# Kernel tuning notes

Measured on AMD Instinct MI355X. Metric: run time of the kernel, lower is better.

## Reference

```python
import jax, jax.numpy as jnp
import numpy as np

N_NODES = 100000
N_EDGES = 1600000
HIDDEN = 128
N_FILTERS = 64
CUTOFF = 8.0
BN_EPS = 1e-3  # keras BatchNormalization default epsilon


def setup_inputs() -> dict:
    key = jax.random.key(0)
    ks = jax.random.split(key, 12)
    x = jax.random.normal(ks[0], (N_NODES, HIDDEN), dtype=jnp.float32)
    edge_index = jax.random.randint(ks[1], (2, N_EDGES), 0, N_NODES, dtype=jnp.int32)
    edge_weight = jax.random.uniform(ks[2], (N_EDGES,), dtype=jnp.float32) * CUTOFF
    edge_attr = jax.random.uniform(ks[3], (N_EDGES, 1), dtype=jnp.float32)
    s = 0.05
    # filter_net: Dense(1->64, tanh), Dense(64->64)
    Wf1 = jax.random.normal(ks[4], (1, N_FILTERS), dtype=jnp.float32) * s
    bf1 = jnp.zeros((N_FILTERS,), jnp.float32)
    Wf2 = jax.random.normal(ks[5], (N_FILTERS, N_FILTERS), dtype=jnp.float32) * s
    bf2 = jnp.zeros((N_FILTERS,), jnp.float32)
    # interaction_net: Dense(128->128, softplus), Dense(128->128)
    Wi1 = jax.random.normal(ks[6], (HIDDEN, HIDDEN), dtype=jnp.float32) * s
    bi1 = jnp.zeros((HIDDEN,), jnp.float32)
    Wi2 = jax.random.normal(ks[7], (HIDDEN, HIDDEN), dtype=jnp.float32) * s
    bi2 = jnp.zeros((HIDDEN,), jnp.float32)
    # BatchNormalization (inference: moving stats)
    gamma = jnp.ones((HIDDEN,), jnp.float32)
    beta = jnp.zeros((HIDDEN,), jnp.float32)
    mov_mean = jax.random.normal(ks[8], (HIDDEN,), dtype=jnp.float32) * 0.01
    mov_var = jnp.ones((HIDDEN,), jnp.float32)
    return {"x": x, "edge_index": edge_index, "edge_weight": edge_weight,
            "edge_attr": edge_attr, "Wf1": Wf1, "bf1": bf1, "Wf2": Wf2, "bf2": bf2,
            "Wi1": Wi1, "bi1": bi1, "Wi2": Wi2, "bi2": bi2,
            "gamma": gamma, "beta": beta, "mov_mean": mov_mean, "mov_var": mov_var}


def reference(x, edge_index, edge_weight, edge_attr, Wf1, bf1, Wf2, bf2,
              Wi1, bi1, Wi2, bi2, gamma, beta, mov_mean, mov_var):
    row, col = edge_index[0], edge_index[1]
    # continuous filters with smooth cosine cutoff
    scaled = edge_weight * (2.0 / CUTOFF) - 1.0                    # [E]
    h = jnp.tanh(scaled[:, None] @ Wf1 + bf1)                      # [E, F]
    filters = h @ Wf2 + bf2                                        # [E, F]
    cut = 0.5 * (jnp.cos(edge_weight * jnp.pi / CUTOFF) + 1.0)
    cut = jnp.where(edge_weight <= CUTOFF, cut, 0.0)               # [E]
    filters = filters * cut[:, None]
    # Original: (neighbor[:, None, :] * filters[:, :, None]).sum(axis=1)
    # == neighbor * filters.sum(-1, keepdims) — same math, no [E,F,H] tensor.
    fsum = jnp.sum(filters, axis=-1, keepdims=True)                # [E, 1]
    messages = x[col] * fsum                                       # [E, H]
    agg = jax.ops.segment_sum(messages, row, num_segments=x.shape[0])  # [N, H]
    out = jax.nn.softplus(agg @ Wi1 + bi1) @ Wi2 + bi2             # [N, H]
    # BatchNormalization, inference mode (training=False)
    out = gamma * (out - mov_mean) * jax.lax.rsqrt(mov_var + BN_EPS) + beta
    return out
```

## Files before the change

### kernel.cpp

```cpp
#include <hip/hip_runtime.h>
#include <math.h>

#define HIDDEN 128
#define NFILT 64
#define SCAN_B 1024
#define LUTK 2048

typedef __attribute__((ext_vector_type(8))) short bf16x8;
typedef __attribute__((ext_vector_type(4))) float f32x4;

__device__ __forceinline__ short f2bf(float f) {
    unsigned u = __float_as_uint(f);
    unsigned r = (u + 0x7fffu + ((u >> 16) & 1u)) >> 16;
    return (short)r;
}
__device__ __forceinline__ float bf2f(unsigned short u) {
    return __uint_as_float(((unsigned)u) << 16);
}

__device__ __forceinline__ float softplus_fast(float v) {
    float e = __builtin_amdgcn_exp2f(v * 1.4426950408889634f);
    float r = 0.69314718055994531f * __builtin_amdgcn_logf(1.0f + e);
    return (v > 80.f) ? v : r;
}

__global__ void wsum_kernel(const float* __restrict__ Wf2, const float* __restrict__ bf2,
                            float* __restrict__ wsum, float* __restrict__ bsum) {
    int j = threadIdx.x;
    float s = 0.f;
    for (int f = 0; f < NFILT; ++f) s += Wf2[j * NFILT + f];
    wsum[j] = s;
    if (j == 0) {
        float b = 0.f;
        for (int f = 0; f < NFILT; ++f) b += bf2[f];
        *bsum = b;
    }
}

__device__ __forceinline__ float edge_coeff(float w,
                                            const float* sW, const float* sB,
                                            const float* sS, float bsum) {
    float s = fmaf(w, 0.25f, -1.0f);
    float acc = bsum;
    #pragma unroll 8
    for (int j = 0; j < NFILT; ++j)
        acc += tanhf(fmaf(s, sW[j], sB[j])) * sS[j];
    float cut = (w <= 8.0f) ? 0.5f * (cosf(w * 0.39269908169872414f) + 1.0f) : 0.0f;
    return acc * cut;
}

__global__ void lut_kernel(const float* __restrict__ Wf1, const float* __restrict__ bf1,
                           const float* __restrict__ wsum, const float* __restrict__ bsum,
                           float* __restrict__ lut) {
    int i = blockIdx.x * 256 + threadIdx.x;
    if (i > LUTK) return;
    float w = 8.0f * (float)i / (float)LUTK;
    lut[i] = edge_coeff(w, Wf1, bf1, wsum, *bsum);
}

__device__ __forceinline__ float lut_eval(const float* sl, float w) {
    float t = w * ((float)LUTK / 8.0f);
    t = fminf(fmaxf(t, 0.f), (float)LUTK);
    int i = (int)t;
    i = min(i, LUTK - 1);
    return fmaf(t - (float)i, sl[i + 1] - sl[i], sl[i]);
}

__global__ void prep_w_kernel(const float* __restrict__ Wi1, const float* __restrict__ Wi2,
                              short* __restrict__ W1T, short* __restrict__ W2T,
                              const float* __restrict__ Wf2, const float* __restrict__ bf2,
                              float* __restrict__ wsum, float* __restrict__ bsum,
                              const float* __restrict__ bi2,
                              const float* __restrict__ gamma, const float* __restrict__ beta,
                              const float* __restrict__ mean, const float* __restrict__ var,
                              float* __restrict__ scf, float* __restrict__ shf) {
    int idx = blockIdx.x * 256 + threadIdx.x;
    const float* src = (idx < 16384) ? Wi1 : Wi2;
    short* dst = (idx < 16384) ? W1T : W2T;
    int i = idx & 16383;
    int k = i >> 7, n = i & 127;
    dst[n * HIDDEN + k] = f2bf(src[i]);

    if (blockIdx.x == 0 && threadIdx.x < 64) {
        int j = threadIdx.x;
        float s = 0.f;
        for (int f = 0; f < NFILT; ++f) s += Wf2[j * NFILT + f];
        wsum[j] = s;
        if (j == 0) {
            float b = 0.f;
            for (int f = 0; f < NFILT; ++f) b += bf2[f];
            *bsum = b;
        }
    }
    if (blockIdx.x == 1 && threadIdx.x < HIDDEN) {
        int j = threadIdx.x;
        float sc = gamma[j] * rsqrtf(var[j] + 1e-3f);
        scf[j] = sc;
        shf[j] = (bi2[j] - mean[j]) * sc + beta[j];
    }
}

__global__ __launch_bounds__(256) void x2bf_count_kernel(
    const float* __restrict__ x, short* __restrict__ xh, int total8,
    const int* __restrict__ rows, int* __restrict__ deg,
    int* __restrict__ rank, int E) {
    int i = blockIdx.x * 256 + threadIdx.x;
    if (i < E) rank[i] = atomicAdd(&deg[rows[i]], 1);
    if (i < total8) {
        const float4 v0 = *(const float4*)&x[(size_t)i * 8];
        const float4 v1 = *(const float4*)&x[(size_t)i * 8 + 4];
        bf16x8 o;
        o[0] = f2bf(v0.x); o[1] = f2bf(v0.y); o[2] = f2bf(v0.z); o[3] = f2bf(v0.w);
        o[4] = f2bf(v1.x); o[5] = f2bf(v1.y); o[6] = f2bf(v1.z); o[7] = f2bf(v1.w);
        *(bf16x8*)&xh[(size_t)i * 8] = o;
    }
}

__global__ void count_rank_kernel(const int* __restrict__ rows, int* __restrict__ deg,
                                  int* __restrict__ rank, int E) {
    int e = blockIdx.x * blockDim.x + threadIdx.x;
    if (e < E) rank[e] = atomicAdd(&deg[rows[e]], 1);
}

__global__ void count_kernel(const int* __restrict__ rows, int* __restrict__ deg, int E) {
    int e = blockIdx.x * blockDim.x + threadIdx.x;
    if (e < E) atomicAdd(&deg[rows[e]], 1);
}

__global__ __launch_bounds__(SCAN_B) void scan_p1(const int* __restrict__ deg,
                                                  int* __restrict__ bsums, int N) {
    __shared__ int red[SCAN_B];
    int i = blockIdx.x * SCAN_B + threadIdx.x;
    red[threadIdx.x] = (i < N) ? deg[i] : 0;
    __syncthreads();
    for (int off = SCAN_B / 2; off > 0; off >>= 1) {
        if (threadIdx.x < off) red[threadIdx.x] += red[threadIdx.x + off];
        __syncthreads();
    }
    if (threadIdx.x == 0) bsums[blockIdx.x] = red[0];
}

__global__ __launch_bounds__(SCAN_B) void scan_p2(int* __restrict__ bsums, int B) {
    __shared__ int part[SCAN_B];
    int t = threadIdx.x;
    part[t] = (t < B) ? bsums[t] : 0;
    __syncthreads();
    for (int off = 1; off < SCAN_B; off <<= 1) {
        int v = (t >= off) ? part[t - off] : 0;
        __syncthreads();
        part[t] += v;
        __syncthreads();
    }
    if (t < B) bsums[t] = (t == 0) ? 0 : part[t - 1];
}

template <bool WRITE_CURSOR>
__global__ __launch_bounds__(SCAN_B) void scan_p3_t(int* __restrict__ deg,
                                                    const int* __restrict__ bsums,
                                                    int* __restrict__ offs, int N) {
    __shared__ int part[SCAN_B];
    int t = threadIdx.x;
    int i = blockIdx.x * SCAN_B + t;
    int d = (i < N) ? deg[i] : 0;
    part[t] = d;
    __syncthreads();
    for (int off = 1; off < SCAN_B; off <<= 1) {
        int v = (t >= off) ? part[t - off] : 0;
        __syncthreads();
        part[t] += v;
        __syncthreads();
    }
    int pre = bsums[blockIdx.x] + part[t] - d;
    if (i < N) {
        offs[i] = pre;
        if (WRITE_CURSOR) deg[i] = pre;
        if (i == N - 1) offs[N] = pre + d;
    }
}

__global__ __launch_bounds__(256) void fill_rank_kernel(
    const int* __restrict__ rows, const int* __restrict__ cols,
    const float* __restrict__ ew, const int* __restrict__ rank,
    const int* __restrict__ offs, const float* __restrict__ lut,
    int2* __restrict__ epack, int E) {
    __shared__ float sl[LUTK + 1];
    for (int i = threadIdx.x; i <= LUTK; i += 256) sl[i] = lut[i];
    __syncthreads();
    int e = blockIdx.x * 256 + threadIdx.x;
    if (e >= E) return;
    float f = lut_eval(sl, ew[e]);
    int pos = offs[rows[e]] + rank[e];
    epack[pos] = make_int2(cols[e], __float_as_int(f));
}

__global__ __launch_bounds__(256) void fill_cursor_kernel(
    const int* __restrict__ rows, const int* __restrict__ cols,
    const float* __restrict__ ew, int* __restrict__ cursor,
    const float* __restrict__ lut, int2* __restrict__ epack, int E) {
    __shared__ float sl[LUTK + 1];
    for (int i = threadIdx.x; i <= LUTK; i += 256) sl[i] = lut[i];
    __syncthreads();
    int e = blockIdx.x * 256 + threadIdx.x;
    if (e >= E) return;
    float f = lut_eval(sl, ew[e]);
    int pos = atomicAdd(&cursor[rows[e]], 1);
    epack[pos] = make_int2(cols[e], __float_as_int(f));
}

__global__ __launch_bounds__(256) void gather_bf_kernel(const int* __restrict__ offs,
                                                        const int2* __restrict__ epack,
                                                        const short* __restrict__ xh,
                                                        short* __restrict__ aggh, int N) {
    int t = threadIdx.x;
    int node = blockIdx.x * 16 + (t >> 4);
    if (node >= N) return;
    int lane = t & 15;
    int s = offs[node], eend = offs[node + 1];

    float a[8];
    #pragma unroll
    for (int j = 0; j < 8; ++j) a[j] = 0.f;

    int i = s;
    for (; i + 4 <= eend; i += 4) {
        int2 p0 = epack[i];
        int2 p1 = epack[i + 1];
        int2 p2 = epack[i + 2];
        int2 p3 = epack[i + 3];
        bf16x8 x0 = *(const bf16x8*)&xh[(size_t)p0.x * HIDDEN + lane * 8];
        bf16x8 x1 = *(const bf16x8*)&xh[(size_t)p1.x * HIDDEN + lane * 8];
        bf16x8 x2 = *(const bf16x8*)&xh[(size_t)p2.x * HIDDEN + lane * 8];
        bf16x8 x3 = *(const bf16x8*)&xh[(size_t)p3.x * HIDDEN + lane * 8];
        float f0 = __int_as_float(p0.y), f1 = __int_as_float(p1.y);
        float f2 = __int_as_float(p2.y), f3 = __int_as_float(p3.y);
        #pragma unroll
        for (int j = 0; j < 8; ++j) a[j] = fmaf(bf2f((unsigned short)x0[j]), f0, a[j]);
        #pragma unroll
        for (int j = 0; j < 8; ++j) a[j] = fmaf(bf2f((unsigned short)x1[j]), f1, a[j]);
        #pragma unroll
        for (int j = 0; j < 8; ++j) a[j] = fmaf(bf2f((unsigned short)x2[j]), f2, a[j]);
        #pragma unroll
        for (int j = 0; j < 8; ++j) a[j] = fmaf(bf2f((unsigned short)x3[j]), f3, a[j]);
    }
    for (; i < eend; ++i) {
        int2 p = epack[i];
        float f = __int_as_float(p.y);
        bf16x8 xv = *(const bf16x8*)&xh[(size_t)p.x * HIDDEN + lane * 8];
        #pragma unroll
        for (int j = 0; j < 8; ++j) a[j] = fmaf(bf2f((unsigned short)xv[j]), f, a[j]);
    }

    bf16x8 o;
    #pragma unroll
    for (int j = 0; j < 8; ++j) o[j] = f2bf(a[j]);
    *(bf16x8*)&aggh[(size_t)node * HIDDEN + lane * 8] = o;
}

__global__ __launch_bounds__(256) void gather_kernel(const int* __restrict__ offs,
                                                     const int2* __restrict__ epack,
                                                     const float* __restrict__ x,
                                                     float* __restrict__ agg, int N) {
    int t = threadIdx.x;
    int node = blockIdx.x * 8 + (t >> 5);
    if (node >= N) return;
    int lane = t & 31;
    int s = offs[node], eend = offs[node + 1];
    float4 acc = make_float4(0.f, 0.f, 0.f, 0.f);
    int i = s;
    for (; i + 2 <= eend; i += 2) {
        int2 p0 = epack[i];
        int2 p1 = epack[i + 1];
        float4 x0 = *(const float4*)&x[(size_t)p0.x * HIDDEN + lane * 4];
        float4 x1 = *(const float4*)&x[(size_t)p1.x * HIDDEN + lane * 4];
        float f0 = __int_as_float(p0.y), f1 = __int_as_float(p1.y);
        acc.x = fmaf(x0.x, f0, acc.x); acc.y = fmaf(x0.y, f0, acc.y);
        acc.z = fmaf(x0.z, f0, acc.z); acc.w = fmaf(x0.w, f0, acc.w);
        acc.x = fmaf(x1.x, f1, acc.x); acc.y = fmaf(x1.y, f1, acc.y);
        acc.z = fmaf(x1.z, f1, acc.z); acc.w = fmaf(x1.w, f1, acc.w);
    }
    for (; i < eend; ++i) {
        int2 p = epack[i];
        float f = __int_as_float(p.y);
        const float4 xv = *(const float4*)&x[(size_t)p.x * HIDDEN + lane * 4];
        acc.x = fmaf(xv.x, f, acc.x);
        acc.y = fmaf(xv.y, f, acc.y);
        acc.z = fmaf(xv.z, f, acc.z);
        acc.w = fmaf(xv.w, f, acc.w);
    }
    *(float4*)&agg[(size_t)node * HIDDEN + lane * 4] = acc;
}

#define HROW 136

#define WSWZ(b) ((b) ^ ((((b) >> 8) & 7) << 4))

__global__ __launch_bounds__(512) void mlp_mfma_bf_kernel(
    const short* __restrict__ aggh, float* __restrict__ io,
    const short* __restrict__ W1T, const short* __restrict__ W2T,
    const float* __restrict__ bi1,
    const float* __restrict__ scf, const float* __restrict__ shf,
    int N) {
    __shared__ short wS[HIDDEN * HIDDEN];
    __shared__ short hS[128 * HROW];

    const int t = threadIdx.x;
    const int wave = t >> 6;
    const int lane = t & 63;
    const int quad = lane >> 4;
    const int m16  = lane & 15;
    const int row0 = blockIdx.x * 128 + wave * 16;
    const int arow = row0 + m16;

    const int swzmask = (m16 & 7) << 4;

    bf16x8 w2r[4];
    {
        const bf16x8* w1v = (const bf16x8*)W1T;
        const bf16x8* w2v = (const bf16x8*)W2T;
        bf16x8 w1r[4];
        #pragma unroll
        for (int j = 0; j < 4; ++j) w1r[j] = w1v[t + 512 * j];
        #pragma unroll
        for (int j = 0; j < 4; ++j) w2r[j] = w2v[t + 512 * j];
        #pragma unroll
        for (int j = 0; j < 4; ++j) {
            int b = (t + 512 * j) * 16;
            *(bf16x8*)((char*)wS + WSWZ(b)) = w1r[j];
        }
    }

    float b1v[8];
    #pragma unroll
    for (int ct = 0; ct < 8; ++ct) b1v[ct] = bi1[ct * 16 + m16];

    f32x4 acc[8];
    #pragma unroll
    for (int ct = 0; ct < 8; ++ct) acc[ct] = (f32x4)(0.f);

    __syncthreads();

    #pragma unroll
    for (int ks = 0; ks < 4; ++ks) {
        bf16x8 a;
        if (arow < N) {
            a = *(const bf16x8*)&aggh[(size_t)arow * HIDDEN + ks * 32 + quad * 8];
        } else {
            #pragma unroll
            for (int j = 0; j < 8; ++j) a[j] = 0;
        }
        const char* bbase = (const char*)wS + m16 * 256 + ((ks * 64 + quad * 16) ^ swzmask);
        #pragma unroll
        for (int ct = 0; ct < 8; ++ct) {
            bf16x8 b = *(const bf16x8*)(bbase + ct * 4096);
            acc[ct] = __builtin_amdgcn_mfma_f32_16x16x32_bf16(a, b, acc[ct], 0, 0, 0);
        }
    }

    #pragma unroll
    for (int ct = 0; ct < 8; ++ct) {
        int col = ct * 16 + m16;
        #pragma unroll
        for (int r = 0; r < 4; ++r) {
            int lrow = wave * 16 + quad * 4 + r;
            float h = softplus_fast(acc[ct][r] + b1v[ct]);
            hS[lrow * HROW + col] = f2bf(h);
        }
        acc[ct] = (f32x4)(0.f);
    }
    __syncthreads();

    #pragma unroll
    for (int j = 0; j < 4; ++j) {
        int b = (t + 512 * j) * 16;
        *(bf16x8*)((char*)wS + WSWZ(b)) = w2r[j];
    }
    __syncthreads();

    float scv[8], shv[8];
    #pragma unroll
    for (int ct = 0; ct < 8; ++ct) {
        scv[ct] = scf[ct * 16 + m16];
        shv[ct] = shf[ct * 16 + m16];
    }

    #pragma unroll
    for (int ks = 0; ks < 4; ++ks) {
        bf16x8 a = *(const bf16x8*)&hS[(wave * 16 + m16) * HROW + ks * 32 + quad * 8];
        const char* bbase = (const char*)wS + m16 * 256 + ((ks * 64 + quad * 16) ^ swzmask);
        #pragma unroll
        for (int ct = 0; ct < 8; ++ct) {
            bf16x8 b = *(const bf16x8*)(bbase + ct * 4096);
            acc[ct] = __builtin_amdgcn_mfma_f32_16x16x32_bf16(a, b, acc[ct], 0, 0, 0);
        }
    }

    #pragma unroll
    for (int r = 0; r < 4; ++r) {
        int grow = row0 + quad * 4 + r;
        if (grow < N) {
            float* p = &io[(size_t)grow * HIDDEN + m16];
            #pragma unroll
            for (int ct = 0; ct < 8; ++ct)
                p[ct * 16] = fmaf(acc[ct][r], scv[ct], shv[ct]);
        }
    }
}

__global__ __launch_bounds__(256) void mlp_mfma_kernel(
    float* io,
    const short* __restrict__ W1T, const short* __restrict__ W2T,
    const float* __restrict__ bi1,
    const float* __restrict__ scf, const float* __restrict__ shf,
    int N) {
    __shared__ short hS[64 * HROW];

    const int t = threadIdx.x;
    const int wave = t >> 6;
    const int lane = t & 63;
    const int quad = lane >> 4;
    const int m16  = lane & 15;
    const int row0 = blockIdx.x * 64 + wave * 16;
    const int arow = row0 + m16;

    f32x4 acc[8];
    #pragma unroll
    for (int ct = 0; ct < 8; ++ct) acc[ct] = (f32x4)(0.f);

    #pragma unroll
    for (int ks = 0; ks < 4; ++ks) {
        bf16x8 a;
        if (arow < N) {
            const float* ap = &io[(size_t)arow * HIDDEN + ks * 32 + quad * 8];
            float4 v0 = *(const float4*)ap;
            float4 v1 = *(const float4*)(ap + 4);
            a[0] = f2bf(v0.x); a[1] = f2bf(v0.y); a[2] = f2bf(v0.z); a[3] = f2bf(v0.w);
            a[4] = f2bf(v1.x); a[5] = f2bf(v1.y); a[6] = f2bf(v1.z); a[7] = f2bf(v1.w);
        } else {
            #pragma unroll
            for (int j = 0; j < 8; ++j) a[j] = 0;
        }
        #pragma unroll
        for (int ct = 0; ct < 8; ++ct) {
            bf16x8 b = *(const bf16x8*)&W1T[(ct * 16 + m16) * HIDDEN + ks * 32 + quad * 8];
            acc[ct] = __builtin_amdgcn_mfma_f32_16x16x32_bf16(a, b, acc[ct], 0, 0, 0);
        }
    }

    #pragma unroll
    for (int ct = 0; ct < 8; ++ct) {
        int col = ct * 16 + m16;
        float b1 = bi1[col];
        #pragma unroll
        for (int r = 0; r < 4; ++r) {
            int lrow = wave * 16 + quad * 4 + r;
            float h = softplus_fast(acc[ct][r] + b1);
            hS[lrow * HROW + col] = f2bf(h);
            acc[ct][r] = 0.f;
        }
    }
    __syncthreads();

    #pragma unroll
    for (int ks = 0; ks < 4; ++ks) {
        bf16x8 a = *(const bf16x8*)&hS[(wave * 16 + m16) * HROW + ks * 32 + quad * 8];
        #pragma unroll
        for (int ct = 0; ct < 8; ++ct) {
            bf16x8 b = *(const bf16x8*)&W2T[(ct * 16 + m16) * HIDDEN + ks * 32 + quad * 8];
            acc[ct] = __builtin_amdgcn_mfma_f32_16x16x32_bf16(a, b, acc[ct], 0, 0, 0);
        }
    }

    #pragma unroll
    for (int ct = 0; ct < 8; ++ct) {
        int col = ct * 16 + m16;
        float sc = scf[col], sh = shf[col];
        #pragma unroll
        for (int r = 0; r < 4; ++r) {
            int grow = row0 + quad * 4 + r;
            if (grow < N)
                io[(size_t)grow * HIDDEN + col] = fmaf(acc[ct][r], sc, sh);
        }
    }
}

__global__ void edge_filter_kernel(const float* __restrict__ ew,
                                   const float* __restrict__ Wf1, const float* __restrict__ bf1,
                                   const float* __restrict__ wsum, const float* __restrict__ bsum,
                                   float* __restrict__ fs, int E) {
    __shared__ float sW[NFILT], sB[NFILT], sS[NFILT];
    if (threadIdx.x < NFILT) {
        sW[threadIdx.x] = Wf1[threadIdx.x];
        sB[threadIdx.x] = bf1[threadIdx.x];
        sS[threadIdx.x] = wsum[threadIdx.x];
    }
    __syncthreads();
    int e = blockIdx.x * blockDim.x + threadIdx.x;
    if (e >= E) return;
    fs[e] = edge_coeff(ew[e], sW, sB, sS, *bsum);
}

__global__ void scatter_kernel(const int* __restrict__ rows, const int* __restrict__ cols,
                               const float* __restrict__ x, const float* __restrict__ fs,
                               float* __restrict__ agg, int E) {
    int t = threadIdx.x;
    int e = blockIdx.x * 8 + (t >> 5);
    if (e >= E) return;
    int lane = t & 31;
    int r = rows[e];
    int c = cols[e];
    float f = fs[e];
    const float4 xv = *(const float4*)&x[c * HIDDEN + lane * 4];
    float* dst = &agg[r * HIDDEN + lane * 4];
    atomicAdd(dst + 0, xv.x * f);
    atomicAdd(dst + 1, xv.y * f);
    atomicAdd(dst + 2, xv.z * f);
    atomicAdd(dst + 3, xv.w * f);
}

__global__ __launch_bounds__(256) void mlp_kernel(
    float* __restrict__ io,
    const float* __restrict__ Wi1, const float* __restrict__ bi1,
    const float* __restrict__ Wi2, const float* __restrict__ bi2,
    const float* __restrict__ gamma, const float* __restrict__ beta,
    const float* __restrict__ mean, const float* __restrict__ var,
    int N) {
    __shared__ float As[64 * HIDDEN];
    __shared__ float Wh[64 * HIDDEN];

    const int t = threadIdx.x;
    const int row0 = blockIdx.x * 64;
    const int col4 = (t & 31) * 4;
    const int rgrp = t >> 5;

    #pragma unroll
    for (int i = 0; i < 8; ++i) {
        int f4 = t + 256 * i;
        int r = f4 >> 5, c4 = (f4 & 31) * 4;
        int node = row0 + r;
        float4 v = make_float4(0.f, 0.f, 0.f, 0.f);
        if (node < N) v = *(const float4*)&io[node * HIDDEN + c4];
        *(float4*)&As[r * HIDDEN + c4] = v;
    }

    float acc[8][4];
    #pragma unroll
    for (int r = 0; r < 8; ++r)
        for (int j = 0; j < 4; ++j) acc[r][j] = 0.f;

    for (int kh = 0; kh < 2; ++kh) {
        __syncthreads();
        #pragma unroll
        for (int i = 0; i < 8; ++i) {
            int f4 = t + 256 * i;
            int kr = f4 >> 5, c4 = (f4 & 31) * 4;
            *(float4*)&Wh[kr * HIDDEN + c4] = *(const float4*)&Wi1[(kh * 64 + kr) * HIDDEN + c4];
        }
        __syncthreads();
        for (int k = 0; k < 64; ++k) {
            float4 w = *(const float4*)&Wh[k * HIDDEN + col4];
            #pragma unroll
            for (int r = 0; r < 8; ++r) {
                float a = As[(rgrp + 8 * r) * HIDDEN + kh * 64 + k];
                acc[r][0] = fmaf(a, w.x, acc[r][0]);
                acc[r][1] = fmaf(a, w.y, acc[r][1]);
                acc[r][2] = fmaf(a, w.z, acc[r][2]);
                acc[r][3] = fmaf(a, w.w, acc[r][3]);
            }
        }
    }
    __syncthreads();

    {
        float4 b = *(const float4*)&bi1[col4];
        float bv[4] = {b.x, b.y, b.z, b.w};
        #pragma unroll
        for (int r = 0; r < 8; ++r) {
            float hv[4];
            #pragma unroll
            for (int j = 0; j < 4; ++j) {
                float v = acc[r][j] + bv[j];
                hv[j] = softplus_fast(v);
                acc[r][j] = 0.f;
            }
            *(float4*)&As[(rgrp + 8 * r) * HIDDEN + col4] =
                make_float4(hv[0], hv[1], hv[2], hv[3]);
        }
    }

    for (int kh = 0; kh < 2; ++kh) {
        __syncthreads();
        #pragma unroll
        for (int i = 0; i < 8; ++i) {
            int f4 = t + 256 * i;
            int kr = f4 >> 5, c4 = (f4 & 31) * 4;
            *(float4*)&Wh[kr * HIDDEN + c4] = *(const float4*)&Wi2[(kh * 64 + kr) * HIDDEN + c4];
        }
        __syncthreads();
        for (int k = 0; k < 64; ++k) {
            float4 w = *(const float4*)&Wh[k * HIDDEN + col4];
            #pragma unroll
            for (int r = 0; r < 8; ++r) {
                float a = As[(rgrp + 8 * r) * HIDDEN + kh * 64 + k];
                acc[r][0] = fmaf(a, w.x, acc[r][0]);
                acc[r][1] = fmaf(a, w.y, acc[r][1]);
                acc[r][2] = fmaf(a, w.z, acc[r][2]);
                acc[r][3] = fmaf(a, w.w, acc[r][3]);
            }
        }
    }

    {
        float4 b2 = *(const float4*)&bi2[col4];
        float4 g  = *(const float4*)&gamma[col4];
        float4 be = *(const float4*)&beta[col4];
        float4 mu = *(const float4*)&mean[col4];
        float4 va = *(const float4*)&var[col4];
        float bv[4]  = {b2.x, b2.y, b2.z, b2.w};
        float gv[4]  = {g.x, g.y, g.z, g.w};
        float bev[4] = {be.x, be.y, be.z, be.w};
        float muv[4] = {mu.x, mu.y, mu.z, mu.w};
        float vav[4] = {va.x, va.y, va.z, va.w};
        float sc[4];
        #pragma unroll
        for (int j = 0; j < 4; ++j) sc[j] = gv[j] * rsqrtf(vav[j] + 1e-3f);
        #pragma unroll
        for (int r = 0; r < 8; ++r) {
            int node = row0 + rgrp + 8 * r;
            if (node < N) {
                float o[4];
                #pragma unroll
                for (int j = 0; j < 4; ++j)
                    o[j] = (acc[r][j] + bv[j] - muv[j]) * sc[j] + bev[j];
                *(float4*)&io[node * HIDDEN + col4] = make_float4(o[0], o[1], o[2], o[3]);
            }
        }
    }
}

extern "C" void kernel_launch(void* const* d_in, const int* in_sizes, int n_in,
                              void* d_out, int out_size, void* d_ws, size_t ws_size,
                              hipStream_t stream) {
    const float* x    = (const float*)d_in[0];
    const int*   ei   = (const int*)d_in[1];
    const float* ew   = (const float*)d_in[2];
    const float* Wf1  = (const float*)d_in[4];
    const float* bf1  = (const float*)d_in[5];
    const float* Wf2  = (const float*)d_in[6];
    const float* bf2  = (const float*)d_in[7];
    const float* Wi1  = (const float*)d_in[8];
    const float* bi1  = (const float*)d_in[9];
    const float* Wi2  = (const float*)d_in[10];
    const float* bi2  = (const float*)d_in[11];
    const float* gam  = (const float*)d_in[12];
    const float* bet  = (const float*)d_in[13];
    const float* mmu  = (const float*)d_in[14];
    const float* mva  = (const float*)d_in[15];

    const int N = in_sizes[0] / HIDDEN;
    const int E = in_sizes[2];
    const int* rows = ei;
    const int* cols = ei + E;

    float* io = (float*)d_out;

    const int B = (N + SCAN_B - 1) / SCAN_B;

    char* ws = (char*)d_ws;
    int*   deg    = (int*)ws;
    int*   offs   = deg + N;
    int*   bsums  = offs + N + 1;
    float* wsumv  = (float*)(bsums + B);
    float* bsumv  = wsumv + NFILT;
    float* lut    = bsumv + 1;
    size_t hdr_ints  = (size_t)(2 * N + 1 + B + NFILT + 1 + LUTK + 1);
    size_t epack_off = ((hdr_ints * 4) + 15) & ~(size_t)15;
    int2*  epack  = (int2*)(ws + epack_off);
    size_t wT_off = (epack_off + (size_t)E * sizeof(int2) + 15) & ~(size_t)15;
    short* W1T    = (short*)(ws + wT_off);
    short* W2T    = W1T + HIDDEN * HIDDEN;
    float* scf    = (float*)(W2T + HIDDEN * HIDDEN);
    float* shf    = scf + HIDDEN;
    size_t base_need = wT_off + 2 * HIDDEN * HIDDEN * sizeof(short) + 2 * HIDDEN * sizeof(float);
    size_t rank_off  = (base_need + 15) & ~(size_t)15;
    int*   rank   = (int*)(ws + rank_off);
    size_t rank_need = rank_off + (size_t)E * sizeof(int);
    size_t xh_off    = (rank_need + 15) & ~(size_t)15;
    short* xh     = (short*)(ws + xh_off);
    short* aggh   = xh + (size_t)N * HIDDEN;
    size_t bf_need = xh_off + 2 * (size_t)N * HIDDEN * sizeof(short);

    if (ws_size >= base_need && B <= SCAN_B) {
        const bool use_rank = (ws_size >= rank_need);
        const bool use_bf   = (ws_size >= bf_need);
        hipMemsetAsync(deg, 0, (size_t)N * sizeof(int), stream);
        prep_w_kernel<<<128, 256, 0, stream>>>(Wi1, Wi2, W1T, W2T,
                                               Wf2, bf2, wsumv, bsumv,
                                               bi2, gam, bet, mmu, mva, scf, shf);
        lut_kernel<<<(LUTK + 256) / 256, 256, 0, stream>>>(Wf1, bf1, wsumv, bsumv, lut);
        if (use_bf) {
            int total8 = N * (HIDDEN / 8);
            int work = (total8 > E) ? total8 : E;
            x2bf_count_kernel<<<(work + 255) / 256, 256, 0, stream>>>(x, xh, total8,
                                                                      rows, deg, rank, E);
        } else if (use_rank) {
            count_rank_kernel<<<(E + 255) / 256, 256, 0, stream>>>(rows, deg, rank, E);
        } else {
            count_kernel<<<(E + 255) / 256, 256, 0, stream>>>(rows, deg, E);
        }
        scan_p1<<<B, SCAN_B, 0, stream>>>(deg, bsums, N);
        scan_p2<<<1, SCAN_B, 0, stream>>>(bsums, B);
        if (use_rank) {
            scan_p3_t<false><<<B, SCAN_B, 0, stream>>>(deg, bsums, offs, N);
            fill_rank_kernel<<<(E + 255) / 256, 256, 0, stream>>>(rows, cols, ew, rank,
                                                                  offs, lut, epack, E);
        } else {
            scan_p3_t<true><<<B, SCAN_B, 0, stream>>>(deg, bsums, offs, N);
            fill_cursor_kernel<<<(E + 255) / 256, 256, 0, stream>>>(rows, cols, ew, deg,
                                                                    lut, epack, E);
        }
        if (use_bf) {
            gather_bf_kernel<<<(N + 15) / 16, 256, 0, stream>>>(offs, epack, xh, aggh, N);
            mlp_mfma_bf_kernel<<<(N + 127) / 128, 512, 0, stream>>>(aggh, io, W1T, W2T,
                                                                    bi1, scf, shf, N);
        } else {
            gather_kernel<<<(N + 7) / 8, 256, 0, stream>>>(offs, epack, x, io, N);
            mlp_mfma_kernel<<<(N + 63) / 64, 256, 0, stream>>>(io, W1T, W2T, bi1, scf, shf, N);
        }
    } else {
        float* fs = (float*)d_ws;
        float* w2 = fs + E;
        float* b2 = w2 + NFILT;
        hipMemsetAsync(d_out, 0, (size_t)out_size * sizeof(float), stream);
        wsum_kernel<<<1, 64, 0, stream>>>(Wf2, bf2, w2, b2);
        edge_filter_kernel<<<(E + 255) / 256, 256, 0, stream>>>(ew, Wf1, bf1, w2, b2, fs, E);
        scatter_kernel<<<(E + 7) / 8, 256, 0, stream>>>(rows, cols, x, fs, io, E);
        mlp_kernel<<<(N + 63) / 64, 256, 0, stream>>>(io, Wi1, bi1, Wi2, bi2,
                                                      gam, bet, mmu, mva, N);
    }
}
```

Measured before the change: 353.1 us.

## Fuse CSR gather into MFMA MLP kernel and add nontemporal loads

Merges the bf16 neighbor gather with the two-layer MFMA MLP, so each wave accumulates 16 nodes' aggregates in registers in MFMA A-fragment layout. This removes the bf16 agg round trip through global memory and one launch. Streaming inputs and the output now use nontemporal loads and stores. In exchange, the gather parallelism changes from 16 lanes per node to 4 lanes per node with 32 accumulators per lane, which raises register pressure and makes load balancing across uneven degrees coarser.

```diff
diff --git a/kernel.cpp b/kernel.cpp
--- a/kernel.cpp
+++ b/kernel.cpp
@@ -8,6 +8,8 @@
 
 typedef __attribute__((ext_vector_type(8))) short bf16x8;
 typedef __attribute__((ext_vector_type(4))) float f32x4;
+typedef __attribute__((ext_vector_type(2))) int i32x2;
+typedef __attribute__((ext_vector_type(4))) float f32x4v;
 
 __device__ __forceinline__ short f2bf(float f) {
     unsigned u = __float_as_uint(f);
@@ -105,13 +107,13 @@
     const int* __restrict__ rows, int* __restrict__ deg,
     int* __restrict__ rank, int E) {
     int i = blockIdx.x * 256 + threadIdx.x;
-    if (i < E) rank[i] = atomicAdd(&deg[rows[i]], 1);
+    if (i < E) rank[i] = atomicAdd(&deg[__builtin_nontemporal_load(&rows[i])], 1);
     if (i < total8) {
-        const float4 v0 = *(const float4*)&x[(size_t)i * 8];
-        const float4 v1 = *(const float4*)&x[(size_t)i * 8 + 4];
+        const f32x4v v0 = __builtin_nontemporal_load((const f32x4v*)&x[(size_t)i * 8]);
+        const f32x4v v1 = __builtin_nontemporal_load((const f32x4v*)&x[(size_t)i * 8 + 4]);
         bf16x8 o;
-        o[0] = f2bf(v0.x); o[1] = f2bf(v0.y); o[2] = f2bf(v0.z); o[3] = f2bf(v0.w);
-        o[4] = f2bf(v1.x); o[5] = f2bf(v1.y); o[6] = f2bf(v1.z); o[7] = f2bf(v1.w);
+        o[0] = f2bf(v0[0]); o[1] = f2bf(v0[1]); o[2] = f2bf(v0[2]); o[3] = f2bf(v0[3]);
+        o[4] = f2bf(v1[0]); o[5] = f2bf(v1[1]); o[6] = f2bf(v1[2]); o[7] = f2bf(v1[3]);
         *(bf16x8*)&xh[(size_t)i * 8] = o;
     }
 }
@@ -188,9 +190,10 @@
     __syncthreads();
     int e = blockIdx.x * 256 + threadIdx.x;
     if (e >= E) return;
-    float f = lut_eval(sl, ew[e]);
-    int pos = offs[rows[e]] + rank[e];
-    epack[pos] = make_int2(cols[e], __float_as_int(f));
+    float f = lut_eval(sl, __builtin_nontemporal_load(&ew[e]));
+    int pos = offs[__builtin_nontemporal_load(&rows[e])] +
+              __builtin_nontemporal_load(&rank[e]);
+    epack[pos] = make_int2(__builtin_nontemporal_load(&cols[e]), __float_as_int(f));
 }
 
 __global__ __launch_bounds__(256) void fill_cursor_kernel(
@@ -207,53 +210,161 @@
     epack[pos] = make_int2(cols[e], __float_as_int(f));
 }
 
-__global__ __launch_bounds__(256) void gather_bf_kernel(const int* __restrict__ offs,
-                                                        const int2* __restrict__ epack,
-                                                        const short* __restrict__ xh,
-                                                        short* __restrict__ aggh, int N) {
-    int t = threadIdx.x;
-    int node = blockIdx.x * 16 + (t >> 4);
-    if (node >= N) return;
-    int lane = t & 15;
-    int s = offs[node], eend = offs[node + 1];
-
-    float a[8];
-    #pragma unroll
-    for (int j = 0; j < 8; ++j) a[j] = 0.f;
+#define HROW 136
+
+#define WSWZ(b) ((b) ^ ((((b) >> 8) & 7) << 4))
+
+__global__ __launch_bounds__(512) void gmlp_kernel(
+    const int* __restrict__ offs, const int2* __restrict__ epack,
+    const short* __restrict__ xh, float* __restrict__ io,
+    const short* __restrict__ W1T, const short* __restrict__ W2T,
+    const float* __restrict__ bi1,
+    const float* __restrict__ scf, const float* __restrict__ shf,
+    int N) {
+    __shared__ short wS[HIDDEN * HIDDEN];
+    __shared__ short hS[128 * HROW];
+
+    const int t = threadIdx.x;
+    const int wave = t >> 6;
+    const int lane = t & 63;
+    const int quad = lane >> 4;
+    const int m16  = lane & 15;
+    const int row0 = blockIdx.x * 128 + wave * 16;
+    const int node = row0 + m16;
+
+    const int swzmask = (m16 & 7) << 4;
+
+    {
+        const bf16x8* w1v = (const bf16x8*)W1T;
+        #pragma unroll
+        for (int j = 0; j < 4; ++j) {
+            bf16x8 v = w1v[t + 512 * j];
+            int b = (t + 512 * j) * 16;
+            *(bf16x8*)((char*)wS + WSWZ(b)) = v;
+        }
+    }
+
+    float a[4][8];
+    #pragma unroll
+    for (int ks = 0; ks < 4; ++ks)
+        #pragma unroll
+        for (int j = 0; j < 8; ++j) a[ks][j] = 0.f;
+
+    int s = 0, e = 0;
+    if (node < N) { s = offs[node]; e = offs[node + 1]; }
+    const short* xbase = xh + quad * 8;
 
     int i = s;
-    for (; i + 4 <= eend; i += 4) {
-        int2 p0 = epack[i];
-        int2 p1 = epack[i + 1];
-        int2 p2 = epack[i + 2];
-        int2 p3 = epack[i + 3];
-        bf16x8 x0 = *(const bf16x8*)&xh[(size_t)p0.x * HIDDEN + lane * 8];
-        bf16x8 x1 = *(const bf16x8*)&xh[(size_t)p1.x * HIDDEN + lane * 8];
-        bf16x8 x2 = *(const bf16x8*)&xh[(size_t)p2.x * HIDDEN + lane * 8];
-        bf16x8 x3 = *(const bf16x8*)&xh[(size_t)p3.x * HIDDEN + lane * 8];
-        float f0 = __int_as_float(p0.y), f1 = __int_as_float(p1.y);
-        float f2 = __int_as_float(p2.y), f3 = __int_as_float(p3.y);
-        #pragma unroll
-        for (int j = 0; j < 8; ++j) a[j] = fmaf(bf2f((unsigned short)x0[j]), f0, a[j]);
-        #pragma unroll
-        for (int j = 0; j < 8; ++j) a[j] = fmaf(bf2f((unsigned short)x1[j]), f1, a[j]);
-        #pragma unroll
-        for (int j = 0; j < 8; ++j) a[j] = fmaf(bf2f((unsigned short)x2[j]), f2, a[j]);
-        #pragma unroll
-        for (int j = 0; j < 8; ++j) a[j] = fmaf(bf2f((unsigned short)x3[j]), f3, a[j]);
-    }
-    for (; i < eend; ++i) {
-        int2 p = epack[i];
-        float f = __int_as_float(p.y);
-        bf16x8 xv = *(const bf16x8*)&xh[(size_t)p.x * HIDDEN + lane * 8];
-        #pragma unroll
-        for (int j = 0; j < 8; ++j) a[j] = fmaf(bf2f((unsigned short)xv[j]), f, a[j]);
-    }
-
-    bf16x8 o;
-    #pragma unroll
-    for (int j = 0; j < 8; ++j) o[j] = f2bf(a[j]);
-    *(bf16x8*)&aggh[(size_t)node * HIDDEN + lane * 8] = o;
+    for (; i + 2 <= e; i += 2) {
+        i32x2 p0 = __builtin_nontemporal_load((const i32x2*)&epack[i]);
+        i32x2 p1 = __builtin_nontemporal_load((const i32x2*)&epack[i + 1]);
+        const short* r0 = xbase + (size_t)p0[0] * HIDDEN;
+        const short* r1 = xbase + (size_t)p1[0] * HIDDEN;
+        bf16x8 c0[4], c1[4];
+        #pragma unroll
+        for (int ks = 0; ks < 4; ++ks) c0[ks] = *(const bf16x8*)(r0 + ks * 32);
+        #pragma unroll
+        for (int ks = 0; ks < 4; ++ks) c1[ks] = *(const bf16x8*)(r1 + ks * 32);
+        float f0 = __int_as_float(p0[1]), f1 = __int_as_float(p1[1]);
+        #pragma unroll
+        for (int ks = 0; ks < 4; ++ks)
+            #pragma unroll
+            for (int j = 0; j < 8; ++j)
+                a[ks][j] = fmaf(bf2f((unsigned short)c0[ks][j]), f0, a[ks][j]);
+        #pragma unroll
+        for (int ks = 0; ks < 4; ++ks)
+            #pragma unroll
+            for (int j = 0; j < 8; ++j)
+                a[ks][j] = fmaf(bf2f((unsigned short)c1[ks][j]), f1, a[ks][j]);
+    }
+    for (; i < e; ++i) {
+        i32x2 p = __builtin_nontemporal_load((const i32x2*)&epack[i]);
+        const short* r0 = xbase + (size_t)p[0] * HIDDEN;
+        float f = __int_as_float(p[1]);
+        #pragma unroll
+        for (int ks = 0; ks < 4; ++ks) {
+            bf16x8 c = *(const bf16x8*)(r0 + ks * 32);
+            #pragma unroll
+            for (int j = 0; j < 8; ++j)
+                a[ks][j] = fmaf(bf2f((unsigned short)c[j]), f, a[ks][j]);
+        }
+    }
+
+    float b1v[8];
+    #pragma unroll
+    for (int ct = 0; ct < 8; ++ct) b1v[ct] = bi1[ct * 16 + m16];
+
+    f32x4 acc[8];
+    #pragma unroll
+    for (int ct = 0; ct < 8; ++ct) acc[ct] = (f32x4)(0.f);
+
+    __syncthreads();
+
+    #pragma unroll
+    for (int ks = 0; ks < 4; ++ks) {
+        bf16x8 af;
+        #pragma unroll
+        for (int j = 0; j < 8; ++j) af[j] = f2bf(a[ks][j]);
+        const char* bbase = (const char*)wS + m16 * 256 + ((ks * 64 + quad * 16) ^ swzmask);
+        #pragma unroll
+        for (int ct = 0; ct < 8; ++ct) {
+            bf16x8 b = *(const bf16x8*)(bbase + ct * 4096);
+            acc[ct] = __builtin_amdgcn_mfma_f32_16x16x32_bf16(af, b, acc[ct], 0, 0, 0);
+        }
+    }
+
+    #pragma unroll
+    for (int ct = 0; ct < 8; ++ct) {
+        int col = ct * 16 + m16;
+        #pragma unroll
+        for (int r = 0; r < 4; ++r) {
+            int lrow = wave * 16 + quad * 4 + r;
+            float h = softplus_fast(acc[ct][r] + b1v[ct]);
+            hS[lrow * HROW + col] = f2bf(h);
+        }
+        acc[ct] = (f32x4)(0.f);
+    }
+    __syncthreads();
+
+    {
+        const bf16x8* w2v = (const bf16x8*)W2T;
+        #pragma unroll
+        for (int j = 0; j < 4; ++j) {
+            bf16x8 v = w2v[t + 512 * j];
+            int b = (t + 512 * j) * 16;
+            *(bf16x8*)((char*)wS + WSWZ(b)) = v;
+        }
+    }
+    __syncthreads();
+
+    float scv[8], shv[8];
+    #pragma unroll
+    for (int ct = 0; ct < 8; ++ct) {
+        scv[ct] = scf[ct * 16 + m16];
+        shv[ct] = shf[ct * 16 + m16];
+    }
+
+    #pragma unroll
+    for (int ks = 0; ks < 4; ++ks) {
+        bf16x8 af = *(const bf16x8*)&hS[(wave * 16 + m16) * HROW + ks * 32 + quad * 8];
+        const char* bbase = (const char*)wS + m16 * 256 + ((ks * 64 + quad * 16) ^ swzmask);
+        #pragma unroll
+        for (int ct = 0; ct < 8; ++ct) {
+            bf16x8 b = *(const bf16x8*)(bbase + ct * 4096);
+            acc[ct] = __builtin_amdgcn_mfma_f32_16x16x32_bf16(af, b, acc[ct], 0, 0, 0);
+        }
+    }
+
+    #pragma unroll
+    for (int r = 0; r < 4; ++r) {
+        int grow = row0 + quad * 4 + r;
+        if (grow < N) {
+            float* p = &io[(size_t)grow * HIDDEN + m16];
+            #pragma unroll
+            for (int ct = 0; ct < 8; ++ct)
+                __builtin_nontemporal_store(fmaf(acc[ct][r], scv[ct], shv[ct]), p + ct * 16);
+        }
+    }
 }
 
 __global__ __launch_bounds__(256) void gather_kernel(const int* __restrict__ offs,
@@ -290,122 +401,6 @@
     *(float4*)&agg[(size_t)node * HIDDEN + lane * 4] = acc;
 }
 
-#define HROW 136
-
-#define WSWZ(b) ((b) ^ ((((b) >> 8) & 7) << 4))
-
-__global__ __launch_bounds__(512) void mlp_mfma_bf_kernel(
-    const short* __restrict__ aggh, float* __restrict__ io,
-    const short* __restrict__ W1T, const short* __restrict__ W2T,
-    const float* __restrict__ bi1,
-    const float* __restrict__ scf, const float* __restrict__ shf,
-    int N) {
-    __shared__ short wS[HIDDEN * HIDDEN];
-    __shared__ short hS[128 * HROW];
-
-    const int t = threadIdx.x;
-    const int wave = t >> 6;
-    const int lane = t & 63;
-    const int quad = lane >> 4;
-    const int m16  = lane & 15;
-    const int row0 = blockIdx.x * 128 + wave * 16;
-    const int arow = row0 + m16;
-
-    const int swzmask = (m16 & 7) << 4;
-
-    bf16x8 w2r[4];
-    {
-        const bf16x8* w1v = (const bf16x8*)W1T;
-        const bf16x8* w2v = (const bf16x8*)W2T;
-        bf16x8 w1r[4];
-        #pragma unroll
-        for (int j = 0; j < 4; ++j) w1r[j] = w1v[t + 512 * j];
-        #pragma unroll
-        for (int j = 0; j < 4; ++j) w2r[j] = w2v[t + 512 * j];
-        #pragma unroll
-        for (int j = 0; j < 4; ++j) {
-            int b = (t + 512 * j) * 16;
-            *(bf16x8*)((char*)wS + WSWZ(b)) = w1r[j];
-        }
-    }
-
-    float b1v[8];
-    #pragma unroll
-    for (int ct = 0; ct < 8; ++ct) b1v[ct] = bi1[ct * 16 + m16];
-
-    f32x4 acc[8];
-    #pragma unroll
-    for (int ct = 0; ct < 8; ++ct) acc[ct] = (f32x4)(0.f);
-
-    __syncthreads();
-
-    #pragma unroll
-    for (int ks = 0; ks < 4; ++ks) {
-        bf16x8 a;
-        if (arow < N) {
-            a = *(const bf16x8*)&aggh[(size_t)arow * HIDDEN + ks * 32 + quad * 8];
-        } else {
-            #pragma unroll
-            for (int j = 0; j < 8; ++j) a[j] = 0;
-        }
-        const char* bbase = (const char*)wS + m16 * 256 + ((ks * 64 + quad * 16) ^ swzmask);
-        #pragma unroll
-        for (int ct = 0; ct < 8; ++ct) {
-            bf16x8 b = *(const bf16x8*)(bbase + ct * 4096);
-            acc[ct] = __builtin_amdgcn_mfma_f32_16x16x32_bf16(a, b, acc[ct], 0, 0, 0);
-        }
-    }
-
-    #pragma unroll
-    for (int ct = 0; ct < 8; ++ct) {
-        int col = ct * 16 + m16;
-        #pragma unroll
-        for (int r = 0; r < 4; ++r) {
-            int lrow = wave * 16 + quad * 4 + r;
-            float h = softplus_fast(acc[ct][r] + b1v[ct]);
-            hS[lrow * HROW + col] = f2bf(h);
-        }
-        acc[ct] = (f32x4)(0.f);
-    }
-    __syncthreads();
-
-    #pragma unroll
-    for (int j = 0; j < 4; ++j) {
-        int b = (t + 512 * j) * 16;
-        *(bf16x8*)((char*)wS + WSWZ(b)) = w2r[j];
-    }
-    __syncthreads();
-
-    float scv[8], shv[8];
-    #pragma unroll
-    for (int ct = 0; ct < 8; ++ct) {
-        scv[ct] = scf[ct * 16 + m16];
-        shv[ct] = shf[ct * 16 + m16];
-    }
-
-    #pragma unroll
-    for (int ks = 0; ks < 4; ++ks) {
-        bf16x8 a = *(const bf16x8*)&hS[(wave * 16 + m16) * HROW + ks * 32 + quad * 8];
-        const char* bbase = (const char*)wS + m16 * 256 + ((ks * 64 + quad * 16) ^ swzmask);
-        #pragma unroll
-        for (int ct = 0; ct < 8; ++ct) {
-            bf16x8 b = *(const bf16x8*)(bbase + ct * 4096);
-            acc[ct] = __builtin_amdgcn_mfma_f32_16x16x32_bf16(a, b, acc[ct], 0, 0, 0);
-        }
-    }
-
-    #pragma unroll
-    for (int r = 0; r < 4; ++r) {
-        int grow = row0 + quad * 4 + r;
-        if (grow < N) {
-            float* p = &io[(size_t)grow * HIDDEN + m16];
-            #pragma unroll
-            for (int ct = 0; ct < 8; ++ct)
-                p[ct * 16] = fmaf(acc[ct][r], scv[ct], shv[ct]);
-        }
-    }
-}
-
 __global__ __launch_bounds__(256) void mlp_mfma_kernel(
     float* io,
     const short* __restrict__ W1T, const short* __restrict__ W2T,
@@ -686,8 +681,7 @@
     size_t rank_need = rank_off + (size_t)E * sizeof(int);
     size_t xh_off    = (rank_need + 15) & ~(size_t)15;
     short* xh     = (short*)(ws + xh_off);
-    short* aggh   = xh + (size_t)N * HIDDEN;
-    size_t bf_need = xh_off + 2 * (size_t)N * HIDDEN * sizeof(short);
+    size_t bf_need = xh_off + (size_t)N * HIDDEN * sizeof(short);
 
     if (ws_size >= base_need && B <= SCAN_B) {
         const bool use_rank = (ws_size >= rank_need);
@@ -719,9 +713,8 @@
                                                                     lut, epack, E);
         }
         if (use_bf) {
-            gather_bf_kernel<<<(N + 15) / 16, 256, 0, stream>>>(offs, epack, xh, aggh, N);
-            mlp_mfma_bf_kernel<<<(N + 127) / 128, 512, 0, stream>>>(aggh, io, W1T, W2T,
-                                                                    bi1, scf, shf, N);
+            gmlp_kernel<<<(N + 127) / 128, 512, 0, stream>>>(offs, epack, xh, io,
+                                                             W1T, W2T, bi1, scf, shf, N);
         } else {
             gather_kernel<<<(N + 7) / 8, 256, 0, stream>>>(offs, epack, x, io, N);
             mlp_mfma_kernel<<<(N + 63) / 64, 256, 0, stream>>>(io, W1T, W2T, bi1, scf, shf, N);
```

After: 372.9 us. 5.6% more time.

## Bucket edges by source column within each row for gather locality

Applied to the files above, without the earlier changes.

Counts edges per (row, column-bucket) using a 16-bucket sub-histogram stored in the aggh scratch, adds a per-row scan kernel, and places edges in CSR sorted by column bucket so gathers of x rows have better cache locality. It also adds nontemporal loads and stores for streaming inputs and outputs. This costs an extra memset of N*16 ints, an additional kernel launch, and more scattered atomics.

```diff
diff --git a/kernel.cpp b/kernel.cpp
--- a/kernel.cpp
+++ b/kernel.cpp
@@ -5,9 +5,12 @@
 #define NFILT 64
 #define SCAN_B 1024
 #define LUTK 2048
+#define BK 16
+#define BSH 13
 
 typedef __attribute__((ext_vector_type(8))) short bf16x8;
 typedef __attribute__((ext_vector_type(4))) float f32x4;
+typedef __attribute__((ext_vector_type(4))) float f32x4v;
 
 __device__ __forceinline__ short f2bf(float f) {
     unsigned u = __float_as_uint(f);
@@ -102,18 +105,45 @@
 
 __global__ __launch_bounds__(256) void x2bf_count_kernel(
     const float* __restrict__ x, short* __restrict__ xh, int total8,
-    const int* __restrict__ rows, int* __restrict__ deg,
-    int* __restrict__ rank, int E) {
+    const int* __restrict__ rows, const int* __restrict__ cols,
+    int* __restrict__ deg2, int* __restrict__ rank, int E) {
     int i = blockIdx.x * 256 + threadIdx.x;
-    if (i < E) rank[i] = atomicAdd(&deg[rows[i]], 1);
+    if (i < E) {
+        int r = __builtin_nontemporal_load(&rows[i]);
+        int c = __builtin_nontemporal_load(&cols[i]);
+        rank[i] = atomicAdd(&deg2[r * BK + (c >> BSH)], 1);
+    }
     if (i < total8) {
-        const float4 v0 = *(const float4*)&x[(size_t)i * 8];
-        const float4 v1 = *(const float4*)&x[(size_t)i * 8 + 4];
+        const f32x4v v0 = __builtin_nontemporal_load((const f32x4v*)&x[(size_t)i * 8]);
+        const f32x4v v1 = __builtin_nontemporal_load((const f32x4v*)&x[(size_t)i * 8 + 4]);
         bf16x8 o;
-        o[0] = f2bf(v0.x); o[1] = f2bf(v0.y); o[2] = f2bf(v0.z); o[3] = f2bf(v0.w);
-        o[4] = f2bf(v1.x); o[5] = f2bf(v1.y); o[6] = f2bf(v1.z); o[7] = f2bf(v1.w);
+        o[0] = f2bf(v0[0]); o[1] = f2bf(v0[1]); o[2] = f2bf(v0[2]); o[3] = f2bf(v0[3]);
+        o[4] = f2bf(v1[0]); o[5] = f2bf(v1[1]); o[6] = f2bf(v1[2]); o[7] = f2bf(v1[3]);
         *(bf16x8*)&xh[(size_t)i * 8] = o;
     }
+}
+
+__global__ __launch_bounds__(256) void rowscan_kernel(int* __restrict__ deg2,
+                                                      int* __restrict__ deg, int N) {
+    int r = blockIdx.x * 256 + threadIdx.x;
+    if (r >= N) return;
+    int4* p = (int4*)&deg2[r * BK];
+    int4 v[BK / 4];
+    #pragma unroll
+    for (int q = 0; q < BK / 4; ++q) v[q] = p[q];
+    int a[BK];
+    #pragma unroll
+    for (int q = 0; q < BK / 4; ++q) {
+        a[q * 4 + 0] = v[q].x; a[q * 4 + 1] = v[q].y;
+        a[q * 4 + 2] = v[q].z; a[q * 4 + 3] = v[q].w;
+    }
+    int s = 0;
+    #pragma unroll
+    for (int k = 0; k < BK; ++k) { int t = a[k]; a[k] = s; s += t; }
+    #pragma unroll
+    for (int q = 0; q < BK / 4; ++q)
+        p[q] = make_int4(a[q * 4 + 0], a[q * 4 + 1], a[q * 4 + 2], a[q * 4 + 3]);
+    deg[r] = s;
 }
 
 __global__ void count_rank_kernel(const int* __restrict__ rows, int* __restrict__ deg,
@@ -178,6 +208,23 @@
     }
 }
 
+__global__ __launch_bounds__(256) void fill_rank_b_kernel(
+    const int* __restrict__ rows, const int* __restrict__ cols,
+    const float* __restrict__ ew, const int* __restrict__ rank,
+    const int* __restrict__ offs, const int* __restrict__ deg2,
+    const float* __restrict__ lut, int2* __restrict__ epack, int E) {
+    __shared__ float sl[LUTK + 1];
+    for (int i = threadIdx.x; i <= LUTK; i += 256) sl[i] = lut[i];
+    __syncthreads();
+    int e = blockIdx.x * 256 + threadIdx.x;
+    if (e >= E) return;
+    float f = lut_eval(sl, __builtin_nontemporal_load(&ew[e]));
+    int r = __builtin_nontemporal_load(&rows[e]);
+    int c = __builtin_nontemporal_load(&cols[e]);
+    int pos = offs[r] + deg2[r * BK + (c >> BSH)] + __builtin_nontemporal_load(&rank[e]);
+    epack[pos] = make_int2(c, __float_as_int(f));
+}
+
 __global__ __launch_bounds__(256) void fill_rank_kernel(
     const int* __restrict__ rows, const int* __restrict__ cols,
     const float* __restrict__ ew, const int* __restrict__ rank,
@@ -188,9 +235,10 @@
     __syncthreads();
     int e = blockIdx.x * 256 + threadIdx.x;
     if (e >= E) return;
-    float f = lut_eval(sl, ew[e]);
-    int pos = offs[rows[e]] + rank[e];
-    epack[pos] = make_int2(cols[e], __float_as_int(f));
+    float f = lut_eval(sl, __builtin_nontemporal_load(&ew[e]));
+    int pos = offs[__builtin_nontemporal_load(&rows[e])] +
+              __builtin_nontemporal_load(&rank[e]);
+    epack[pos] = make_int2(__builtin_nontemporal_load(&cols[e]), __float_as_int(f));
 }
 
 __global__ __launch_bounds__(256) void fill_cursor_kernel(
@@ -401,7 +449,7 @@
             float* p = &io[(size_t)grow * HIDDEN + m16];
             #pragma unroll
             for (int ct = 0; ct < 8; ++ct)
-                p[ct * 16] = fmaf(acc[ct][r], scv[ct], shv[ct]);
+                __builtin_nontemporal_store(fmaf(acc[ct][r], scv[ct], shv[ct]), p + ct * 16);
         }
     }
 }
@@ -687,12 +735,18 @@
     size_t xh_off    = (rank_need + 15) & ~(size_t)15;
     short* xh     = (short*)(ws + xh_off);
     short* aggh   = xh + (size_t)N * HIDDEN;
+    int*   deg2   = (int*)aggh;
     size_t bf_need = xh_off + 2 * (size_t)N * HIDDEN * sizeof(short);
 
     if (ws_size >= base_need && B <= SCAN_B) {
         const bool use_rank = (ws_size >= rank_need);
-        const bool use_bf   = (ws_size >= bf_need);
-        hipMemsetAsync(deg, 0, (size_t)N * sizeof(int), stream);
+        const bool use_bf   = (ws_size >= bf_need) &&
+                              ((size_t)N * HIDDEN * sizeof(short) >= (size_t)N * BK * sizeof(int));
+        if (use_bf) {
+            hipMemsetAsync(deg2, 0, (size_t)N * BK * sizeof(int), stream);
+        } else {
+            hipMemsetAsync(deg, 0, (size_t)N * sizeof(int), stream);
+        }
         prep_w_kernel<<<128, 256, 0, stream>>>(Wi1, Wi2, W1T, W2T,
                                                Wf2, bf2, wsumv, bsumv,
                                                bi2, gam, bet, mmu, mva, scf, shf);
@@ -701,7 +755,9 @@
             int total8 = N * (HIDDEN / 8);
             int work = (total8 > E) ? total8 : E;
             x2bf_count_kernel<<<(work + 255) / 256, 256, 0, stream>>>(x, xh, total8,
-                                                                      rows, deg, rank, E);
+                                                                      rows, cols, deg2,
+                                                                      rank, E);
+            rowscan_kernel<<<(N + 255) / 256, 256, 0, stream>>>(deg2, deg, N);
         } else if (use_rank) {
             count_rank_kernel<<<(E + 255) / 256, 256, 0, stream>>>(rows, deg, rank, E);
         } else {
@@ -709,20 +765,24 @@
         }
         scan_p1<<<B, SCAN_B, 0, stream>>>(deg, bsums, N);
         scan_p2<<<1, SCAN_B, 0, stream>>>(bsums, B);
-        if (use_rank) {
+        if (use_bf) {
+            scan_p3_t<false><<<B, SCAN_B, 0, stream>>>(deg, bsums, offs, N);
+            fill_rank_b_kernel<<<(E + 255) / 256, 256, 0, stream>>>(rows, cols, ew, rank,
+                                                                    offs, deg2, lut,
+                                                                    epack, E);
+            gather_bf_kernel<<<(N + 15) / 16, 256, 0, stream>>>(offs, epack, xh, aggh, N);
+            mlp_mfma_bf_kernel<<<(N + 127) / 128, 512, 0, stream>>>(aggh, io, W1T, W2T,
+                                                                    bi1, scf, shf, N);
+        } else if (use_rank) {
             scan_p3_t<false><<<B, SCAN_B, 0, stream>>>(deg, bsums, offs, N);
             fill_rank_kernel<<<(E + 255) / 256, 256, 0, stream>>>(rows, cols, ew, rank,
                                                                   offs, lut, epack, E);
+            gather_kernel<<<(N + 7) / 8, 256, 0, stream>>>(offs, epack, x, io, N);
+            mlp_mfma_kernel<<<(N + 63) / 64, 256, 0, stream>>>(io, W1T, W2T, bi1, scf, shf, N);
         } else {
             scan_p3_t<true><<<B, SCAN_B, 0, stream>>>(deg, bsums, offs, N);
             fill_cursor_kernel<<<(E + 255) / 256, 256, 0, stream>>>(rows, cols, ew, deg,
                                                                     lut, epack, E);
-        }
-        if (use_bf) {
-            gather_bf_kernel<<<(N + 15) / 16, 256, 0, stream>>>(offs, epack, xh, aggh, N);
-            mlp_mfma_bf_kernel<<<(N + 127) / 128, 512, 0, stream>>>(aggh, io, W1T, W2T,
-                                                                    bi1, scf, shf, N);
-        } else {
             gather_kernel<<<(N + 7) / 8, 256, 0, stream>>>(offs, epack, x, io, N);
             mlp_mfma_kernel<<<(N + 63) / 64, 256, 0, stream>>>(io, W1T, W2T, bi1, scf, shf, N);
         }
```

Result: slower. 381.9 us (+8.2%).
